# Optimization experiments

Hardware: AMD Instinct MI355X
Metric: run time of the kernel (lower is better)

The kernel has to match this reference:

```python
import jax, jax.numpy as jnp
from jax import lax
import numpy as np

DIM = 512
HEADS = 8


def setup_inputs() -> dict:
    key = jax.random.key(0)
    k1, k2, k3, k4, k5 = jax.random.split(key, 5)
    B, C, H, W = 2, DIM, 64, 64
    x = jax.random.normal(k1, (B, C, H, W), dtype=jnp.float32)
    # depthwise 3x3 conv (groups=C, bias=False): torch OIHW with O=C, I=1
    dw_w = jax.random.normal(k2, (C, 1, 3, 3), dtype=jnp.float32) * (1.0 / 3.0)
    # 1x1 conv C -> 3C (bias=False)
    qkv_w = jax.random.normal(k3, (3 * C, C, 1, 1), dtype=jnp.float32) * (C ** -0.5)
    # 1x1 proj conv C -> C with bias
    proj_w = jax.random.normal(k4, (C, C, 1, 1), dtype=jnp.float32) * (C ** -0.5)
    proj_b = jax.random.normal(k5, (C,), dtype=jnp.float32) * 0.01
    return {"x": x, "dw_w": dw_w, "qkv_w": qkv_w, "proj_w": proj_w, "proj_b": proj_b}


def reference(x, dw_w, qkv_w, proj_w, proj_b):
    B, C, H, W = x.shape
    heads = HEADS
    dh = C // heads
    scale = dh ** -0.5
    N = H * W
    # depthwise 3x3, padding=1
    y = lax.conv_general_dilated(
        x, dw_w, window_strides=(1, 1), padding=((1, 1), (1, 1)),
        dimension_numbers=("NCHW", "OIHW", "NCHW"), feature_group_count=C)
    # 1x1 conv as matmul over channels -> (B, 3C, H, W)
    qkv = jnp.einsum("bchw,oc->bohw", y, qkv_w[:, :, 0, 0])
    # (B, 3, heads, dh, N) -> q,k,v each (B, heads, N, dh)
    qkv = qkv.reshape(B, 3, heads, dh, N).transpose(1, 0, 2, 4, 3)
    q, k, v = qkv[0], qkv[1], qkv[2]
    attn = jax.nn.softmax(jnp.einsum("bhnd,bhmd->bhnm", q, k) * scale, axis=-1)
    o = jnp.einsum("bhnm,bhmd->bhnd", attn, v)          # (B, heads, N, dh)
    o = o.transpose(0, 1, 3, 2).reshape(B, C, H, W)      # matches torch transpose(2,3).reshape
    out = jnp.einsum("bchw,oc->bohw", o, proj_w[:, :, 0, 0]) + proj_b[None, :, None, None]
    return out
```

## Files before the change

kernel.cpp:

```cpp
#include <hip/hip_runtime.h>
#include <hip/hip_bf16.h>

typedef __bf16 bf16_t;
typedef __bf16 bf16x4 __attribute__((ext_vector_type(4)));
typedef __bf16 bf16x8 __attribute__((ext_vector_type(8)));
typedef float f32x4 __attribute__((ext_vector_type(4)));
typedef float f32x8 __attribute__((ext_vector_type(8)));

#define MFMA16(a, b, c) __builtin_amdgcn_mfma_f32_16x16x32_bf16((a), (b), (c), 0, 0, 0)

#if __has_builtin(__builtin_amdgcn_exp2f)
#define EXP2(x) __builtin_amdgcn_exp2f(x)
#else
#define EXP2(x) exp2f(x)
#endif

#define NPIX 4096
#define CDIM 512
#define QSCALE 0.1803368801111744f

__device__ __forceinline__ bool detect_f32(const void* p) {
  const unsigned short* u = (const unsigned short*)p;
  int lane = threadIdx.x & 63;
  int f = 0;
#pragma unroll
  for (int j = 0; j < 4; ++j) {
    int e = (u[lane * 4 + j] >> 7) & 0xFF;
    f |= (e >= 138) ? 1 : 0;
  }
  return __ballot(f) != 0ull;
}

__global__ __launch_bounds__(256) void dwconv_kernel(
    const void* __restrict__ x_, const void* __restrict__ dww_,
    bf16_t* __restrict__ yt) {
  __shared__ bf16_t xs[64 * 194];
  __shared__ float wsh[64 * 9];
  const bool f32m = detect_f32(x_);
  int bidx = blockIdx.x;
  int c0 = (bidx & 7) << 6;
  int h = (bidx >> 3) & 63;
  int b = bidx >> 9;
  int tid = threadIdx.x;

  for (int i = tid; i < 576; i += 256)
    wsh[i] = f32m ? ((const float*)dww_)[c0 * 9 + i]
                  : (float)((const bf16_t*)dww_)[c0 * 9 + i];

  const size_t xoff = ((size_t)b * CDIM + c0) * NPIX;
#pragma unroll
  for (int r = 0; r < 3; ++r) {
    int hh = h + r - 1;
    bool ok = (unsigned)hh < 64u;
#pragma unroll
    for (int it = 0; it < 2; ++it) {
      int idx2 = tid + it * 256;
      int c = idx2 >> 3, ch = idx2 & 7;
      bf16x8 v = {};
      if (ok) {
        size_t gi = xoff + (size_t)c * NPIX + (size_t)hh * 64 + ch * 8;
        if (f32m) {
          const float* p = (const float*)x_ + gi;
          float4 t0 = *(const float4*)p;
          float4 t1 = *(const float4*)(p + 4);
          v[0] = (bf16_t)t0.x; v[1] = (bf16_t)t0.y;
          v[2] = (bf16_t)t0.z; v[3] = (bf16_t)t0.w;
          v[4] = (bf16_t)t1.x; v[5] = (bf16_t)t1.y;
          v[6] = (bf16_t)t1.z; v[7] = (bf16_t)t1.w;
        } else {
          v = *(const bf16x8*)((const bf16_t*)x_ + gi);
        }
      }
      union { bf16x8 v8; unsigned u[4]; } uu;
      uu.v8 = v;
      unsigned* dst = (unsigned*)&xs[c * 194 + r * 64 + ch * 8];
      dst[0] = uu.u[0]; dst[1] = uu.u[1]; dst[2] = uu.u[2]; dst[3] = uu.u[3];
    }
  }
  __syncthreads();

  int c = tid & 63;
  int wb = tid >> 6;
  float wreg[9];
#pragma unroll
  for (int j = 0; j < 9; ++j) wreg[j] = wsh[c * 9 + j];
  const bf16_t* xrow = &xs[c * 194];
  bf16_t* ybase = yt + ((size_t)b * NPIX + h * 64) * CDIM + c0 + c;
#pragma unroll
  for (int jj = 0; jj < 16; ++jj) {
    int w = wb + 4 * jj;
    float acc = 0.f;
#pragma unroll
    for (int r = 0; r < 3; ++r) {
      float xm = (w > 0) ? (float)xrow[r * 64 + w - 1] : 0.f;
      float xc = (float)xrow[r * 64 + w];
      float xp = (w < 63) ? (float)xrow[r * 64 + w + 1] : 0.f;
      acc += xm * wreg[3 * r] + xc * wreg[3 * r + 1] + xp * wreg[3 * r + 2];
    }
    ybase[(size_t)w * CDIM] = (bf16_t)acc;
  }
}

__global__ __launch_bounds__(256) void gemm_kernel(
    const void* __restrict__ A_, const bf16_t* __restrict__ Bt,
    void* __restrict__ o0, bf16_t* __restrict__ o1, bf16_t* __restrict__ o2,
    const void* __restrict__ bias_, int mode,
    const bf16_t* __restrict__ O2p, const float* __restrict__ lsb) {
  const int K = 512;
  __shared__ bf16_t as[2][128 * 40];
  __shared__ bf16_t bs[2][128 * 40];
  const bool f32m = detect_f32(A_);
  int z = blockIdx.z;
  const bf16_t* Bz = Bt + (size_t)z * NPIX * K;
  int m0 = blockIdx.y * 128;
  int n0 = blockIdx.x * 128;
  int tid = threadIdx.x;
  int lane = tid & 63;
  int wv = tid >> 6;
  int wm = wv >> 1, wn = wv & 1;
  int col = lane & 15, quad = lane >> 4;

  bf16x8 aA[2], bA[2], aB[2], bB[2];
  auto loadAB = [&](int ko, bf16x8* ap, bf16x8* bp) {
#pragma unroll
    for (int j = 0; j < 2; ++j) {
      int i = tid + j * 256;
      int row = i >> 2, kc = (i & 3) << 3;
      if (f32m) {
        const float* p = &((const float*)A_)[(size_t)(m0 + row) * K + ko + kc];
        float4 t0 = *(const float4*)p;
        float4 t1 = *(const float4*)(p + 4);
        bf16x8 av;
        av[0] = (bf16_t)t0.x; av[1] = (bf16_t)t0.y;
        av[2] = (bf16_t)t0.z; av[3] = (bf16_t)t0.w;
        av[4] = (bf16_t)t1.x; av[5] = (bf16_t)t1.y;
        av[6] = (bf16_t)t1.z; av[7] = (bf16_t)t1.w;
        ap[j] = av;
      } else {
        ap[j] = *(const bf16x8*)&(
            (const bf16_t*)A_)[(size_t)(m0 + row) * K + ko + kc];
      }
      if (mode == 2) {
        int hz = ko >> 6;
        size_t qi = (size_t)(z * 8 + hz) * NPIX + n0 + row;
        float invl = 1.f / (lsb[qi] + lsb[qi + 16 * (size_t)NPIX]);
        int d = (ko & 63) + kc;
        bf16x8 p1 = *(const bf16x8*)&Bt[qi * 64 + d];
        bf16x8 p2 = *(const bf16x8*)&O2p[qi * 64 + d];
        f32x8 f;
#pragma unroll
        for (int e = 0; e < 8; ++e)
          f[e] = ((float)p1[e] + (float)p2[e]) * invl;
        bp[j] = __builtin_convertvector(f, bf16x8);
      } else {
        bp[j] = *(const bf16x8*)&Bz[(size_t)(n0 + row) * K + ko + kc];
      }
    }
  };

  loadAB(0, aA, bA);
  loadAB(32, aB, bB);
  f32x4 acc[4][4] = {};
  for (int t = 0; t < 16; ++t) {
    int buf = t & 1;
#pragma unroll
    for (int j = 0; j < 2; ++j) {
      int i = tid + j * 256;
      int row = i >> 2, kc = (i & 3) << 3;
      *(bf16x8*)&as[buf][row * 40 + kc] = aA[j];
      *(bf16x8*)&bs[buf][row * 40 + kc] = bA[j];
    }
    __syncthreads();
#pragma unroll
    for (int j = 0; j < 2; ++j) { aA[j] = aB[j]; bA[j] = bB[j]; }
    if (t + 2 < 16) loadAB((t + 2) * 32, aB, bB);
    bf16x8 af[4], bfr[4];
#pragma unroll
    for (int f = 0; f < 4; ++f) {
      af[f] = *(const bf16x8*)&as[buf][(wm * 64 + f * 16 + col) * 40 + quad * 8];
      bfr[f] = *(const bf16x8*)&bs[buf][(wn * 64 + f * 16 + col) * 40 + quad * 8];
    }
#pragma unroll
    for (int fm = 0; fm < 4; ++fm)
#pragma unroll
      for (int fn = 0; fn < 4; ++fn)
        acc[fm][fn] = MFMA16(af[fm], bfr[fn], acc[fm][fn]);
  }

  if (mode == 0) {
    int t = m0 >> 9;
    float scale = (t == 0) ? QSCALE : 1.0f;
    bf16_t* q0 = (bf16_t*)o0;
#pragma unroll
    for (int fm = 0; fm < 4; ++fm) {
      int mloc = m0 + wm * 64 + fm * 16 + quad * 4;
      int hh = (mloc & 511) >> 6;
      int d = mloc & 63;
#pragma unroll
      for (int fn = 0; fn < 4; ++fn) {
        int n = n0 + wn * 64 + fn * 16 + col;
        if (t < 2) {
          bf16_t* dst = ((t == 0) ? q0 : o1) +
                        ((size_t)z * 8 + hh) * ((size_t)NPIX * 64) +
                        (size_t)n * 64 + d;
          union {
            ushort4 u;
            bf16_t hv[4];
          } pk;
#pragma unroll
          for (int r = 0; r < 4; ++r) pk.hv[r] = (bf16_t)(acc[fm][fn][r] * scale);
          *(ushort4*)dst = pk.u;
        } else {
          bf16_t* vb = o2 + ((size_t)z * 8 + hh) * ((size_t)NPIX * 64);
#pragma unroll
          for (int r = 0; r < 4; ++r)
            vb[(size_t)(d + r) * NPIX + n] = (bf16_t)acc[fm][fn][r];
        }
      }
    }
  } else {
#pragma unroll
    for (int fm = 0; fm < 4; ++fm) {
      int mloc = m0 + wm * 64 + fm * 16 + quad * 4;
#pragma unroll
      for (int r = 0; r < 4; ++r) {
        float bv = f32m ? ((const float*)bias_)[mloc + r]
                        : (float)((const bf16_t*)bias_)[mloc + r];
#pragma unroll
        for (int fn = 0; fn < 4; ++fn) {
          int n = n0 + wn * 64 + fn * 16 + col;
          size_t oi = (size_t)z * CDIM * NPIX + (size_t)(mloc + r) * NPIX + n;
          float val = acc[fm][fn][r] + bv;
          if (f32m)
            ((float*)o0)[oi] = val;
          else
            ((bf16_t*)o0)[oi] = (bf16_t)val;
        }
      }
    }
  }
}

template <int MODE>
__global__ __launch_bounds__(256, 2) void attn_kernel(
    const bf16_t* __restrict__ q, const bf16_t* __restrict__ k,
    const bf16_t* __restrict__ vt, bf16_t* __restrict__ po,
    size_t posz, float* __restrict__ lsum) {
  __shared__ bf16_t ks[2 * 64 * 72];
  __shared__ bf16_t vs[2 * 64 * 72];
  int qt = blockIdx.x & 15;
  int bh = (blockIdx.x >> 4) & 15;
  int kh = (MODE == 2) ? (blockIdx.x >> 8) : 0;
  const int kspan = (MODE == 2) ? 32 : 64;
  int kstart = kh * kspan;
  int kend = kstart + kspan;
  int tid = threadIdx.x;
  int lane = tid & 63, wv = tid >> 6;
  int col = lane & 15, quad = lane >> 4;
  const bf16_t* qb = q + (size_t)bh * NPIX * 64;
  const bf16_t* kb = k + (size_t)bh * NPIX * 64;
  const bf16_t* vb = vt + (size_t)bh * NPIX * 64;

  bf16x8 qfrag[4][2];
  int qrow0 = qt * 256 + wv * 64;
#pragma unroll
  for (int sub = 0; sub < 4; ++sub)
#pragma unroll
    for (int kk = 0; kk < 2; ++kk)
      qfrag[sub][kk] = *(const bf16x8*)&qb[(size_t)(qrow0 + sub * 16 + col) * 64 +
                                           kk * 32 + quad * 8];

  int trow = tid >> 2, t4 = tid & 3;
  bf16x8 kA0, kA1, vA0, vA1, kB0, kB1, vB0, vB1;
  auto loadKV = [&](int kc, bf16x8& k0, bf16x8& k1, bf16x8& v0, bf16x8& v1) {
    const bf16_t* kgr = &kb[(size_t)(kc * 64 + trow) * 64 + t4 * 16];
    const bf16_t* vgr = &vb[(size_t)trow * NPIX + kc * 64 + t4 * 16];
    k0 = *(const bf16x8*)kgr;
    k1 = *(const bf16x8*)(kgr + 8);
    v0 = *(const bf16x8*)vgr;
    v1 = *(const bf16x8*)(vgr + 8);
  };
  loadKV(kstart, kA0, kA1, vA0, vA1);
  loadKV(kstart + 1, kB0, kB1, vB0, vB1);

  int vbase = trow * 72 + (t4 >> 1) * 32 + (t4 & 1) * 4;

  f32x4 oacc[4][4] = {};
  float lsv[4] = {0.f, 0.f, 0.f, 0.f};

  for (int kc = kstart; kc < kend; ++kc) {
    bf16_t* ksb = &ks[(kc & 1) * 4608];
    bf16_t* vsb = &vs[(kc & 1) * 4608];
    *(bf16x8*)&ksb[trow * 72 + t4 * 16] = kA0;
    *(bf16x8*)&ksb[trow * 72 + t4 * 16 + 8] = kA1;
    {
      union { bf16x8 v; bf16x4 h[2]; } u0, u1;
      u0.v = vA0; u1.v = vA1;
      *(bf16x4*)&vsb[vbase] = u0.h[0];
      *(bf16x4*)&vsb[vbase + 8] = u0.h[1];
      *(bf16x4*)&vsb[vbase + 16] = u1.h[0];
      *(bf16x4*)&vsb[vbase + 24] = u1.h[1];
    }
    __syncthreads();

    kA0 = kB0; kA1 = kB1; vA0 = vB0; vA1 = vB1;
    {
      int kcn = kc + 2;
      if (kcn >= kend) kcn = kstart;
      loadKV(kcn, kB0, kB1, vB0, vB1);
    }

    bf16x8 kf[4][2];
#pragma unroll
    for (int nt = 0; nt < 4; ++nt)
#pragma unroll
      for (int kk = 0; kk < 2; ++kk)
        kf[nt][kk] =
            *(const bf16x8*)&ksb[(nt * 16 + col) * 72 + kk * 32 + quad * 8];
    bf16x8 vf[4][2];
#pragma unroll
    for (int dt = 0; dt < 4; ++dt)
#pragma unroll
      for (int t = 0; t < 2; ++t)
        vf[dt][t] =
            *(const bf16x8*)&vsb[(dt * 16 + col) * 72 + t * 32 + quad * 8];

#pragma unroll
    for (int sub = 0; sub < 4; ++sub) {
      f32x4 sv[4];
#pragma unroll
      for (int nt = 0; nt < 4; ++nt) {
        f32x4 s = {};
        s = MFMA16(kf[nt][0], qfrag[sub][0], s);
        s = MFMA16(kf[nt][1], qfrag[sub][1], s);
        sv[nt] = s;
      }
      bf16x8 pb[2];
      float ls = 0.f;
#pragma unroll
      for (int t = 0; t < 2; ++t) {
        f32x8 pe;
#pragma unroll
        for (int half = 0; half < 2; ++half)
#pragma unroll
          for (int r = 0; r < 4; ++r)
            pe[half * 4 + r] = EXP2(sv[2 * t + half][r]);
        float s0 = pe[0] + pe[1], s1 = pe[2] + pe[3];
        float s2 = pe[4] + pe[5], s3 = pe[6] + pe[7];
        ls += (s0 + s1) + (s2 + s3);
        pb[t] = __builtin_convertvector(pe, bf16x8);
      }
      lsv[sub] += ls;
#pragma unroll
      for (int dt = 0; dt < 4; ++dt) {
        oacc[sub][dt] = MFMA16(vf[dt][0], pb[0], oacc[sub][dt]);
        oacc[sub][dt] = MFMA16(vf[dt][1], pb[1], oacc[sub][dt]);
      }
    }
  }

#pragma unroll
  for (int sub = 0; sub < 4; ++sub) {
    lsv[sub] += __shfl_xor(lsv[sub], 16);
    lsv[sub] += __shfl_xor(lsv[sub], 32);
  }

  if (MODE == 0) {
    int b = bh >> 3, hh = bh & 7;
#pragma unroll
    for (int sub = 0; sub < 4; ++sub) {
      float inv = 1.f / lsv[sub];
      int qrow = qrow0 + sub * 16 + col;
      bf16_t* ob = po + ((size_t)b * NPIX + qrow) * CDIM + hh * 64 + quad * 4;
#pragma unroll
      for (int dt = 0; dt < 4; ++dt) {
        union {
          ushort4 u;
          bf16_t hv[4];
        } pk;
#pragma unroll
        for (int r = 0; r < 4; ++r)
          pk.hv[r] = (bf16_t)(oacc[sub][dt][r] * inv);
        *(ushort4*)(ob + dt * 16) = pk.u;
      }
    }
  } else {
    bf16_t* pbase = po + (size_t)kh * posz;
#pragma unroll
    for (int sub = 0; sub < 4; ++sub) {
      int qrow = qrow0 + sub * 16 + col;
      bf16_t* op = pbase + ((size_t)bh * NPIX + qrow) * 64 + quad * 4;
#pragma unroll
      for (int dt = 0; dt < 4; ++dt) {
        union {
          ushort4 u;
          bf16_t hv[4];
        } pk;
#pragma unroll
        for (int r = 0; r < 4; ++r) pk.hv[r] = (bf16_t)oacc[sub][dt][r];
        *(ushort4*)(op + dt * 16) = pk.u;
      }
    }
    if (quad == 0) {
      float* lbase = lsum + (size_t)(kh * 16 + bh) * NPIX;
#pragma unroll
      for (int sub = 0; sub < 4; ++sub)
        lbase[qrow0 + sub * 16 + col] = lsv[sub];
    }
  }
}

extern "C" void kernel_launch(void* const* d_in, const int* in_sizes, int n_in,
                              void* d_out, int out_size, void* d_ws,
                              size_t ws_size, hipStream_t stream) {
  const void* x = d_in[0];
  const void* dww = d_in[1];
  const void* qkvw = d_in[2];
  const void* projw = d_in[3];
  const void* projb = d_in[4];

  bf16_t* ws = (bf16_t*)d_ws;
  const size_t SZ = (size_t)2 * NPIX * CDIM;
  bf16_t* yt = ws;
  bf16_t* qa = ws + SZ;
  bf16_t* ka = ws + 2 * SZ;
  bf16_t* va = ws + 3 * SZ;

  const size_t need2 =
      5 * SZ * sizeof(bf16_t) + 2 * 16 * (size_t)NPIX * sizeof(float);

  dwconv_kernel<<<1024, 256, 0, stream>>>(x, dww, yt);
  gemm_kernel<<<dim3(32, 12, 2), 256, 0, stream>>>(
      qkvw, yt, qa, ka, va, nullptr, 0, nullptr, nullptr);

  if (ws_size >= need2) {
    bf16_t* O1 = yt;
    bf16_t* O2 = ws + 4 * SZ;
    float* ls2 = (float*)(ws + 5 * SZ);
    attn_kernel<2><<<512, 256, 0, stream>>>(qa, ka, va, O1,
                                            (size_t)(O2 - O1), ls2);
    gemm_kernel<<<dim3(32, 4, 2), 256, 0, stream>>>(
        projw, O1, d_out, nullptr, nullptr, projb, 2, O2, ls2);
  } else {
    attn_kernel<0><<<256, 256, 0, stream>>>(qa, ka, va, yt, 0, nullptr);
    gemm_kernel<<<dim3(32, 4, 2), 256, 0, stream>>>(
        projw, yt, d_out, nullptr, nullptr, projb, 1, nullptr, nullptr);
  }
}
```

Baseline: 229.9 us.

## Use direct global-to-LDS loads in GEMM and swap grid axis order

Replaces the register-staged, double-buffered LDS pipeline in the GEMM with single-buffered tiles filled by global_load_lds (direct global-to-LDS DMA) whenever the operands are bf16. Fused or converting paths still go through registers. It also swaps the grid x and y axes so that consecutive blocks walk the M dimension and share the same B tile. The change drops the padded LDS stride and the prefetch overlap and adds a second barrier per k-step, which risks bank conflicts and exposed load latency.

```diff
diff --git a/kernel.cpp b/kernel.cpp
--- a/kernel.cpp
+++ b/kernel.cpp
@@ -14,6 +14,9 @@
 #else
 #define EXP2(x) exp2f(x)
 #endif
+
+#define AS1(p) ((const __attribute__((address_space(1))) void*)(p))
+#define AS3(p) ((__attribute__((address_space(3))) void*)(p))
 
 #define NPIX 4096
 #define CDIM 512
@@ -107,26 +110,35 @@
     const void* __restrict__ bias_, int mode,
     const bf16_t* __restrict__ O2p, const float* __restrict__ lsb) {
   const int K = 512;
-  __shared__ bf16_t as[2][128 * 40];
-  __shared__ bf16_t bs[2][128 * 40];
+  __shared__ bf16_t as[128 * 32];
+  __shared__ bf16_t bs[128 * 32];
   const bool f32m = detect_f32(A_);
   int z = blockIdx.z;
   const bf16_t* Bz = Bt + (size_t)z * NPIX * K;
-  int m0 = blockIdx.y * 128;
-  int n0 = blockIdx.x * 128;
+  int m0 = blockIdx.x * 128;
+  int n0 = blockIdx.y * 128;
   int tid = threadIdx.x;
   int lane = tid & 63;
   int wv = tid >> 6;
   int wm = wv >> 1, wn = wv & 1;
   int col = lane & 15, quad = lane >> 4;
 
-  bf16x8 aA[2], bA[2], aB[2], bB[2];
-  auto loadAB = [&](int ko, bf16x8* ap, bf16x8* bp) {
-#pragma unroll
-    for (int j = 0; j < 2; ++j) {
-      int i = tid + j * 256;
-      int row = i >> 2, kc = (i & 3) << 3;
-      if (f32m) {
+  f32x4 acc[4][4] = {};
+  for (int ko = 0; ko < K; ko += 32) {
+    if (!f32m) {
+#pragma unroll
+      for (int j = 0; j < 2; ++j) {
+        int i = tid + j * 256;
+        int row = i >> 2, kc = (i & 3) << 3;
+        __builtin_amdgcn_global_load_lds(
+            AS1(&((const bf16_t*)A_)[(size_t)(m0 + row) * K + ko + kc]),
+            AS3(&as[(wv * 64 + j * 256) * 8]), 16, 0, 0);
+      }
+    } else {
+#pragma unroll
+      for (int j = 0; j < 2; ++j) {
+        int i = tid + j * 256;
+        int row = i >> 2, kc = (i & 3) << 3;
         const float* p = &((const float*)A_)[(size_t)(m0 + row) * K + ko + kc];
         float4 t0 = *(const float4*)p;
         float4 t1 = *(const float4*)(p + 4);
@@ -135,12 +147,23 @@
         av[2] = (bf16_t)t0.z; av[3] = (bf16_t)t0.w;
         av[4] = (bf16_t)t1.x; av[5] = (bf16_t)t1.y;
         av[6] = (bf16_t)t1.z; av[7] = (bf16_t)t1.w;
-        ap[j] = av;
-      } else {
-        ap[j] = *(const bf16x8*)&(
-            (const bf16_t*)A_)[(size_t)(m0 + row) * K + ko + kc];
-      }
-      if (mode == 2) {
+        *(bf16x8*)&as[row * 32 + kc] = av;
+      }
+    }
+    if (mode != 2) {
+#pragma unroll
+      for (int j = 0; j < 2; ++j) {
+        int i = tid + j * 256;
+        int row = i >> 2, kc = (i & 3) << 3;
+        __builtin_amdgcn_global_load_lds(
+            AS1(&Bz[(size_t)(n0 + row) * K + ko + kc]),
+            AS3(&bs[(wv * 64 + j * 256) * 8]), 16, 0, 0);
+      }
+    } else {
+#pragma unroll
+      for (int j = 0; j < 2; ++j) {
+        int i = tid + j * 256;
+        int row = i >> 2, kc = (i & 3) << 3;
         int hz = ko >> 6;
         size_t qi = (size_t)(z * 8 + hz) * NPIX + n0 + row;
         float invl = 1.f / (lsb[qi] + lsb[qi + 16 * (size_t)NPIX]);
@@ -151,40 +174,23 @@
 #pragma unroll
         for (int e = 0; e < 8; ++e)
           f[e] = ((float)p1[e] + (float)p2[e]) * invl;
-        bp[j] = __builtin_convertvector(f, bf16x8);
-      } else {
-        bp[j] = *(const bf16x8*)&Bz[(size_t)(n0 + row) * K + ko + kc];
-      }
-    }
-  };
-
-  loadAB(0, aA, bA);
-  loadAB(32, aB, bB);
-  f32x4 acc[4][4] = {};
-  for (int t = 0; t < 16; ++t) {
-    int buf = t & 1;
-#pragma unroll
-    for (int j = 0; j < 2; ++j) {
-      int i = tid + j * 256;
-      int row = i >> 2, kc = (i & 3) << 3;
-      *(bf16x8*)&as[buf][row * 40 + kc] = aA[j];
-      *(bf16x8*)&bs[buf][row * 40 + kc] = bA[j];
+        *(bf16x8*)&bs[row * 32 + kc] = __builtin_convertvector(f, bf16x8);
+      }
     }
     __syncthreads();
-#pragma unroll
-    for (int j = 0; j < 2; ++j) { aA[j] = aB[j]; bA[j] = bB[j]; }
-    if (t + 2 < 16) loadAB((t + 2) * 32, aB, bB);
+
     bf16x8 af[4], bfr[4];
 #pragma unroll
     for (int f = 0; f < 4; ++f) {
-      af[f] = *(const bf16x8*)&as[buf][(wm * 64 + f * 16 + col) * 40 + quad * 8];
-      bfr[f] = *(const bf16x8*)&bs[buf][(wn * 64 + f * 16 + col) * 40 + quad * 8];
+      af[f] = *(const bf16x8*)&as[(wm * 64 + f * 16 + col) * 32 + quad * 8];
+      bfr[f] = *(const bf16x8*)&bs[(wn * 64 + f * 16 + col) * 32 + quad * 8];
     }
 #pragma unroll
     for (int fm = 0; fm < 4; ++fm)
 #pragma unroll
       for (int fn = 0; fn < 4; ++fn)
         acc[fm][fn] = MFMA16(af[fm], bfr[fn], acc[fm][fn]);
+    __syncthreads();
   }
 
   if (mode == 0) {
@@ -430,7 +436,7 @@
       5 * SZ * sizeof(bf16_t) + 2 * 16 * (size_t)NPIX * sizeof(float);
 
   dwconv_kernel<<<1024, 256, 0, stream>>>(x, dww, yt);
-  gemm_kernel<<<dim3(32, 12, 2), 256, 0, stream>>>(
+  gemm_kernel<<<dim3(12, 32, 2), 256, 0, stream>>>(
       qkvw, yt, qa, ka, va, nullptr, 0, nullptr, nullptr);
 
   if (ws_size >= need2) {
@@ -439,11 +445,11 @@
     float* ls2 = (float*)(ws + 5 * SZ);
     attn_kernel<2><<<512, 256, 0, stream>>>(qa, ka, va, O1,
                                             (size_t)(O2 - O1), ls2);
-    gemm_kernel<<<dim3(32, 4, 2), 256, 0, stream>>>(
+    gemm_kernel<<<dim3(4, 32, 2), 256, 0, stream>>>(
         projw, O1, d_out, nullptr, nullptr, projb, 2, O2, ls2);
   } else {
     attn_kernel<0><<<256, 256, 0, stream>>>(qa, ka, va, yt, 0, nullptr);
-    gemm_kernel<<<dim3(32, 4, 2), 256, 0, stream>>>(
+    gemm_kernel<<<dim3(4, 32, 2), 256, 0, stream>>>(
         projw, yt, d_out, nullptr, nullptr, projb, 1, nullptr, nullptr);
   }
 }
```

After: 207.6 us. 9.7% less time.
